# Kernel optimization log

Hardware: AMD Instinct MI355X
Metric: run time of the kernel (lower is better)

Reference implementation:

```python
import jax, jax.numpy as jnp
import numpy as np

LEARNING_RATE = 0.01


def setup_inputs() -> dict:
    key = jax.random.key(0)
    k1, k2 = jax.random.split(key)
    O, D = 512, 128  # output_dim, input_dim; batch must equal output_dim for the broadcast
    x = jax.random.normal(k1, (O, D), dtype=jnp.float32)
    weights = jax.random.normal(k2, (O, O, D), dtype=jnp.float32)
    return {"x": x, "weights": weights}


def reference(x, weights):
    # x: (B, D) with B == O; weights: (O, O, D)
    O = weights.shape[0]
    sigma = O / 2.0
    x = x.reshape(-1, weights.shape[-1])
    diff = weights - x[:, None, :]                      # (O, O, D)
    distances = jnp.sum(diff * diff, axis=-1)            # (O, O)
    winner = jnp.argmin(distances, axis=1)               # (O,)
    neighborhood = jnp.exp(-distances / (2.0 * sigma ** 2))  # (O, O)
    delta = LEARNING_RATE * neighborhood[..., None] * (x[:, None, :] - weights)  # (O, O, D)
    # torch: self.weights.data += torch.sum(delta, dim=0)  -> (O, D) broadcast over rows
    new_weights = weights + jnp.sum(delta, axis=0)        # (O, O, D)
    return winner, new_weights
```

## Files before the change

### kernel.cpp

```cpp
#include <hip/hip_runtime.h>
#include <stdint.h>

#define O_DIM 512
#define D_DIM 128
#define LR 0.01f
#define INV2SIG2 7.62939453125e-6f

typedef float f32x4 __attribute__((ext_vector_type(4)));

__global__ __launch_bounds__(256) void som_fused(
    const float* __restrict__ X,
    const float* __restrict__ W,
    float* __restrict__ dist,
    float* __restrict__ outW)
{
    const int j    = blockIdx.x;
    const int wave = threadIdx.x >> 6;
    const int lane = threadIdx.x & 63;
    const int g    = lane >> 4;
    const int i16  = lane & 15;
    const int dA   = i16 * 4;
    const int dB   = 64 + dA;

    float acc[8];
    #pragma unroll
    for (int u = 0; u < 8; ++u) acc[u] = 0.f;

    const int bbase = wave * 4 + g;

    #pragma unroll 2
    for (int k = 0; k < 32; k += 4) {
        float4 wa[4], wb[4], xa[4], xb[4];
        int bb[4];
        #pragma unroll
        for (int u = 0; u < 4; ++u) {
            bb[u] = bbase + (k + u) * 16;
            const float* wrow = W + ((size_t)bb[u] * O_DIM + j) * D_DIM;
            const float* xrow = X + (size_t)bb[u] * D_DIM;
            wa[u] = *(const float4*)(wrow + dA);
            wb[u] = *(const float4*)(wrow + dB);
            xa[u] = *(const float4*)(xrow + dA);
            xb[u] = *(const float4*)(xrow + dB);
        }
        #pragma unroll
        for (int u = 0; u < 4; ++u) {
            float dx[8];
            dx[0] = wa[u].x - xa[u].x; dx[1] = wa[u].y - xa[u].y;
            dx[2] = wa[u].z - xa[u].z; dx[3] = wa[u].w - xa[u].w;
            dx[4] = wb[u].x - xb[u].x; dx[5] = wb[u].y - xb[u].y;
            dx[6] = wb[u].z - xb[u].z; dx[7] = wb[u].w - xb[u].w;

            float s = 0.f;
            #pragma unroll
            for (int v = 0; v < 8; ++v) s = fmaf(dx[v], dx[v], s);
            s += __shfl_xor(s, 1, 64);
            s += __shfl_xor(s, 2, 64);
            s += __shfl_xor(s, 4, 64);
            s += __shfl_xor(s, 8, 64);

            if (i16 == 0) dist[(size_t)bb[u] * O_DIM + j] = s;

            const float c = LR * __expf(-s * INV2SIG2);
            #pragma unroll
            for (int v = 0; v < 8; ++v) acc[v] = fmaf(-c, dx[v], acc[v]);
        }
    }

    #pragma unroll
    for (int u = 0; u < 8; ++u) {
        acc[u] += __shfl_xor(acc[u], 16, 64);
        acc[u] += __shfl_xor(acc[u], 32, 64);
    }

    __shared__ float sacc[4][D_DIM];
    __shared__ float sS[D_DIM];
    if (g == 0) {
        #pragma unroll
        for (int u = 0; u < 4; ++u) {
            sacc[wave][dA + u] = acc[u];
            sacc[wave][dB + u] = acc[4 + u];
        }
    }
    __syncthreads();
    if (threadIdx.x < D_DIM) {
        const int d = threadIdx.x;
        sS[d] = sacc[0][d] + sacc[1][d] + sacc[2][d] + sacc[3][d];
    }
    __syncthreads();

    const f32x4 sA = *(const f32x4*)(sS + dA);
    const f32x4 sB = *(const f32x4*)(sS + dB);

    #pragma unroll 4
    for (int k = 0; k < 32; ++k) {
        const int b = bbase + k * 16;
        const size_t e = ((size_t)b * O_DIM + j) * D_DIM;
        const f32x4 w4a = *(const f32x4*)(W + e + dA);
        const f32x4 w4b = *(const f32x4*)(W + e + dB);
        __builtin_nontemporal_store(w4a + sA, (f32x4*)(outW + e + dA));
        __builtin_nontemporal_store(w4b + sB, (f32x4*)(outW + e + dB));
    }
}

__global__ __launch_bounds__(64) void som_argmin(
    const float* __restrict__ dist,
    float* __restrict__ out)
{
    const int b = blockIdx.x;
    const int lane = threadIdx.x;
    unsigned long long best = ~0ull;
    #pragma unroll
    for (int k = 0; k < 8; ++k) {
        const int jj = k * 64 + lane;
        const float s = dist[(size_t)b * O_DIM + jj];
        const unsigned long long key =
            ((unsigned long long)__float_as_uint(s) << 32) | (unsigned int)jj;
        best = key < best ? key : best;
    }
    #pragma unroll
    for (int m = 32; m >= 1; m >>= 1) {
        const unsigned long long o = __shfl_xor(best, m, 64);
        best = o < best ? o : best;
    }
    if (lane == 0) out[b] = (float)(unsigned int)(best & 0xFFFFFFFFull);
}


__global__ __launch_bounds__(256) void som_pass1_atomic(
    const float* __restrict__ X, const float* __restrict__ W,
    float* __restrict__ S, unsigned long long* __restrict__ wkey)
{
    const int j = blockIdx.x >> 2, chunk = blockIdx.x & 3;
    const int wave = threadIdx.x >> 6, lane = threadIdx.x & 63;
    const int d0 = lane * 2;
    float accx = 0.f, accy = 0.f;
    const int b_end = chunk * 128 + 128;
    for (int b = chunk * 128 + wave; b < b_end; b += 4) {
        const float2 w2 = *(const float2*)(W + ((size_t)b * O_DIM + j) * D_DIM + d0);
        const float2 x2 = *(const float2*)(X + (size_t)b * D_DIM + d0);
        const float dx = w2.x - x2.x, dy = w2.y - x2.y;
        float s = dx * dx + dy * dy;
        #pragma unroll
        for (int m = 32; m >= 1; m >>= 1) s += __shfl_xor(s, m, 64);
        if (lane == 0)
            atomicMin(&wkey[b], ((unsigned long long)__float_as_uint(s) << 32) | (unsigned)j);
        const float c = LR * __expf(-s * INV2SIG2);
        accx -= c * dx; accy -= c * dy;
    }
    __shared__ float sacc[D_DIM];
    if (threadIdx.x < D_DIM) sacc[threadIdx.x] = 0.f;
    __syncthreads();
    atomicAdd(&sacc[d0], accx); atomicAdd(&sacc[d0 + 1], accy);
    __syncthreads();
    if (threadIdx.x < D_DIM) atomicAdd(&S[(size_t)j * D_DIM + threadIdx.x], sacc[threadIdx.x]);
}

__global__ __launch_bounds__(256) void som_pass2_atomic(
    const float* __restrict__ W, const float* __restrict__ S,
    const unsigned long long* __restrict__ wkey, float* __restrict__ out)
{
    const size_t tid = (size_t)blockIdx.x * blockDim.x + threadIdx.x;
    if (tid < O_DIM) out[tid] = (float)(unsigned int)(wkey[tid] & 0xFFFFFFFFull);
    float* __restrict__ outW = out + O_DIM;
    const size_t total4 = (size_t)O_DIM * O_DIM * D_DIM / 4;
    const size_t stride = (size_t)gridDim.x * blockDim.x;
    for (size_t i = tid; i < total4; i += stride) {
        const size_t e = i * 4;
        const float4 w4 = *(const float4*)(W + e);
        const float4 s4 = *(const float4*)(S + (e & (size_t)(O_DIM * D_DIM - 1)));
        float4 o4 = {w4.x + s4.x, w4.y + s4.y, w4.z + s4.z, w4.w + s4.w};
        *(float4*)(outW + e) = o4;
    }
}

extern "C" void kernel_launch(void* const* d_in, const int* in_sizes, int n_in,
                              void* d_out, int out_size, void* d_ws, size_t ws_size,
                              hipStream_t stream)
{
    const float* X = (const float*)d_in[0];
    const float* W = (const float*)d_in[1];
    float* out = (float*)d_out;

    const size_t DIST_BYTES = (size_t)O_DIM * O_DIM * sizeof(float);

    if (ws_size >= DIST_BYTES) {
        float* dist = (float*)d_ws;
        som_fused <<<dim3(512), dim3(256), 0, stream>>>(X, W, dist, out + O_DIM);
        som_argmin<<<dim3(512), dim3(64),  0, stream>>>(dist, out);
    } else {
        float* S = (float*)d_ws;
        unsigned long long* wkey =
            (unsigned long long*)((char*)d_ws + (size_t)O_DIM * D_DIM * sizeof(float));
        hipMemsetAsync(S, 0, (size_t)O_DIM * D_DIM * sizeof(float), stream);
        hipMemsetAsync(wkey, 0xFF, (size_t)O_DIM * sizeof(unsigned long long), stream);
        som_pass1_atomic<<<dim3(2048), dim3(256), 0, stream>>>(X, W, S, wkey);
        som_pass2_atomic<<<dim3(2048), dim3(256), 0, stream>>>(W, S, wkey, out);
    }
}
```

Before: 65.58 us.

## Split fused SOM kernel into two passes over half-batch blocks, merging argmin into pass B

The single fused kernel, which ran 512 blocks, each computing distances and then writing its column, is replaced by two kernels of 1024 blocks. Each block handles half of the batch rows, and partial update sums go through a workspace buffer. The argmin is folded into the second pass rather than launched as its own kernel. This doubles the block count for better occupancy and drops a launch. The cost is that W is read once more from global memory across kernels rather than while still warm within one block.

```diff
diff --git a/kernel.cpp b/kernel.cpp
--- a/kernel.cpp
+++ b/kernel.cpp
@@ -8,13 +8,14 @@
 
 typedef float f32x4 __attribute__((ext_vector_type(4)));
 
-__global__ __launch_bounds__(256) void som_fused(
+__global__ __launch_bounds__(256) void som_passA(
     const float* __restrict__ X,
     const float* __restrict__ W,
     float* __restrict__ dist,
-    float* __restrict__ outW)
-{
-    const int j    = blockIdx.x;
+    float* __restrict__ Spart)
+{
+    const int j    = blockIdx.x >> 1;
+    const int h    = blockIdx.x & 1;
     const int wave = threadIdx.x >> 6;
     const int lane = threadIdx.x & 63;
     const int g    = lane >> 4;
@@ -26,15 +27,15 @@
     #pragma unroll
     for (int u = 0; u < 8; ++u) acc[u] = 0.f;
 
-    const int bbase = wave * 4 + g;
-
-    #pragma unroll 2
-    for (int k = 0; k < 32; k += 4) {
+    const int bbase = h * 256 + wave * 4 + g;
+
+    #pragma unroll
+    for (int kb = 0; kb < 4; ++kb) {
         float4 wa[4], wb[4], xa[4], xb[4];
         int bb[4];
         #pragma unroll
         for (int u = 0; u < 4; ++u) {
-            bb[u] = bbase + (k + u) * 16;
+            bb[u] = bbase + (kb * 4 + u) * 16;
             const float* wrow = W + ((size_t)bb[u] * O_DIM + j) * D_DIM;
             const float* xrow = X + (size_t)bb[u] * D_DIM;
             wa[u] = *(const float4*)(wrow + dA);
@@ -73,7 +74,6 @@
     }
 
     __shared__ float sacc[4][D_DIM];
-    __shared__ float sS[D_DIM];
     if (g == 0) {
         #pragma unroll
         for (int u = 0; u < 4; ++u) {
@@ -84,15 +84,56 @@
     __syncthreads();
     if (threadIdx.x < D_DIM) {
         const int d = threadIdx.x;
-        sS[d] = sacc[0][d] + sacc[1][d] + sacc[2][d] + sacc[3][d];
-    }
-    __syncthreads();
-
-    const f32x4 sA = *(const f32x4*)(sS + dA);
-    const f32x4 sB = *(const f32x4*)(sS + dB);
-
+        Spart[((size_t)j * 2 + h) * D_DIM + d] =
+            sacc[0][d] + sacc[1][d] + sacc[2][d] + sacc[3][d];
+    }
+}
+
+__global__ __launch_bounds__(256) void som_passB(
+    const float* __restrict__ W,
+    const float* __restrict__ dist,
+    const float* __restrict__ Spart,
+    float* __restrict__ out)
+{
+    const int j = blockIdx.x >> 1;
+    const int h = blockIdx.x & 1;
+    const int t = threadIdx.x;
+    float* __restrict__ outW = out + O_DIM;
+
+    if (blockIdx.x < O_DIM && t < 64) {
+        const int b = blockIdx.x;
+        unsigned long long best = ~0ull;
+        #pragma unroll
+        for (int k = 0; k < 8; ++k) {
+            const int jj = k * 64 + t;
+            const float s = dist[(size_t)b * O_DIM + jj];
+            const unsigned long long key =
+                ((unsigned long long)__float_as_uint(s) << 32) | (unsigned int)jj;
+            best = key < best ? key : best;
+        }
+        #pragma unroll
+        for (int m = 32; m >= 1; m >>= 1) {
+            const unsigned long long o = __shfl_xor(best, m, 64);
+            best = o < best ? o : best;
+        }
+        if (t == 0) out[b] = (float)(unsigned int)(best & 0xFFFFFFFFull);
+    }
+
+    const int wave = t >> 6;
+    const int lane = t & 63;
+    const int g    = lane >> 4;
+    const int i16  = lane & 15;
+    const int dA   = i16 * 4;
+    const int dB   = 64 + dA;
+
+    const float* sp0 = Spart + ((size_t)j * 2) * D_DIM;
+    const float* sp1 = sp0 + D_DIM;
+    const f32x4 sA = *(const f32x4*)(sp0 + dA) + *(const f32x4*)(sp1 + dA);
+    const f32x4 sB = *(const f32x4*)(sp0 + dB) + *(const f32x4*)(sp1 + dB);
+
+    const int bbase = h * 256 + wave * 4 + g;
     #pragma unroll 4
-    for (int k = 0; k < 32; ++k) {
+    for (int k = 0; k < 16; ++k) {
         const int b = bbase + k * 16;
         const size_t e = ((size_t)b * O_DIM + j) * D_DIM;
         const f32x4 w4a = *(const f32x4*)(W + e + dA);
@@ -100,29 +141,6 @@
         __builtin_nontemporal_store(w4a + sA, (f32x4*)(outW + e + dA));
         __builtin_nontemporal_store(w4b + sB, (f32x4*)(outW + e + dB));
     }
-}
-
-__global__ __launch_bounds__(64) void som_argmin(
-    const float* __restrict__ dist,
-    float* __restrict__ out)
-{
-    const int b = blockIdx.x;
-    const int lane = threadIdx.x;
-    unsigned long long best = ~0ull;
-    #pragma unroll
-    for (int k = 0; k < 8; ++k) {
-        const int jj = k * 64 + lane;
-        const float s = dist[(size_t)b * O_DIM + jj];
-        const unsigned long long key =
-            ((unsigned long long)__float_as_uint(s) << 32) | (unsigned int)jj;
-        best = key < best ? key : best;
-    }
-    #pragma unroll
-    for (int m = 32; m >= 1; m >>= 1) {
-        const unsigned long long o = __shfl_xor(best, m, 64);
-        best = o < best ? o : best;
-    }
-    if (lane == 0) out[b] = (float)(unsigned int)(best & 0xFFFFFFFFull);
 }
 
 
@@ -181,12 +199,14 @@
     const float* W = (const float*)d_in[1];
     float* out = (float*)d_out;
 
-    const size_t DIST_BYTES = (size_t)O_DIM * O_DIM * sizeof(float);
-
-    if (ws_size >= DIST_BYTES) {
-        float* dist = (float*)d_ws;
-        som_fused <<<dim3(512), dim3(256), 0, stream>>>(X, W, dist, out + O_DIM);
-        som_argmin<<<dim3(512), dim3(64),  0, stream>>>(dist, out);
+    const size_t DIST_BYTES  = (size_t)O_DIM * O_DIM * sizeof(float);
+    const size_t SPART_BYTES = 2ull * O_DIM * D_DIM * sizeof(float);
+
+    if (ws_size >= DIST_BYTES + SPART_BYTES) {
+        float* dist  = (float*)d_ws;
+        float* Spart = (float*)((char*)d_ws + DIST_BYTES);
+        som_passA<<<dim3(1024), dim3(256), 0, stream>>>(X, W, dist, Spart);
+        som_passB<<<dim3(1024), dim3(256), 0, stream>>>(W, dist, Spart, out);
     } else {
         float* S = (float*)d_ws;
         unsigned long long* wkey =
```

After: 67.64 us. 3.1% more time.

## Hold weight slice in registers across both passes with 1024-thread blocks

Applied to the files above, without the earlier changes.

The fused kernel now uses 1024 threads per block, and each thread loads its 16 weight vectors into registers once. Those registers feed both the distance/neighborhood pass and the final update store, so the second global read of W is gone. The cost is higher register pressure (16 f32x4 per thread) at 1024-thread blocks, which may limit occupancy, plus a larger 16-way shared reduction.

```diff
diff --git a/kernel.cpp b/kernel.cpp
--- a/kernel.cpp
+++ b/kernel.cpp
@@ -8,97 +8,73 @@
 
 typedef float f32x4 __attribute__((ext_vector_type(4)));
 
-__global__ __launch_bounds__(256) void som_fused(
+__global__ __launch_bounds__(1024) void som_fused(
     const float* __restrict__ X,
     const float* __restrict__ W,
     float* __restrict__ dist,
     float* __restrict__ outW)
 {
     const int j    = blockIdx.x;
-    const int wave = threadIdx.x >> 6;
-    const int lane = threadIdx.x & 63;
-    const int g    = lane >> 4;
-    const int i16  = lane & 15;
-    const int dA   = i16 * 4;
-    const int dB   = 64 + dA;
+    const int t    = threadIdx.x;
+    const int wave = t >> 6;
+    const int lane = t & 63;
+    const int g    = lane >> 5;
+    const int i32  = lane & 31;
+    const int d0   = i32 * 4;
+    const int brow = wave * 2 + g;
 
-    float acc[8];
+    f32x4 wv[16];
     #pragma unroll
-    for (int u = 0; u < 8; ++u) acc[u] = 0.f;
-
-    const int bbase = wave * 4 + g;
-
-    #pragma unroll 2
-    for (int k = 0; k < 32; k += 4) {
-        float4 wa[4], wb[4], xa[4], xb[4];
-        int bb[4];
-        #pragma unroll
-        for (int u = 0; u < 4; ++u) {
-            bb[u] = bbase + (k + u) * 16;
-            const float* wrow = W + ((size_t)bb[u] * O_DIM + j) * D_DIM;
-            const float* xrow = X + (size_t)bb[u] * D_DIM;
-            wa[u] = *(const float4*)(wrow + dA);
-            wb[u] = *(const float4*)(wrow + dB);
-            xa[u] = *(const float4*)(xrow + dA);
-            xb[u] = *(const float4*)(xrow + dB);
-        }
-        #pragma unroll
-        for (int u = 0; u < 4; ++u) {
-            float dx[8];
-            dx[0] = wa[u].x - xa[u].x; dx[1] = wa[u].y - xa[u].y;
-            dx[2] = wa[u].z - xa[u].z; dx[3] = wa[u].w - xa[u].w;
-            dx[4] = wb[u].x - xb[u].x; dx[5] = wb[u].y - xb[u].y;
-            dx[6] = wb[u].z - xb[u].z; dx[7] = wb[u].w - xb[u].w;
-
-            float s = 0.f;
-            #pragma unroll
-            for (int v = 0; v < 8; ++v) s = fmaf(dx[v], dx[v], s);
-            s += __shfl_xor(s, 1, 64);
-            s += __shfl_xor(s, 2, 64);
-            s += __shfl_xor(s, 4, 64);
-            s += __shfl_xor(s, 8, 64);
-
-            if (i16 == 0) dist[(size_t)bb[u] * O_DIM + j] = s;
-
-            const float c = LR * __expf(-s * INV2SIG2);
-            #pragma unroll
-            for (int v = 0; v < 8; ++v) acc[v] = fmaf(-c, dx[v], acc[v]);
-        }
+    for (int s = 0; s < 16; ++s) {
+        const int b = s * 32 + brow;
+        wv[s] = *(const f32x4*)(W + ((size_t)b * O_DIM + j) * D_DIM + d0);
     }
 
+    f32x4 acc = {0.f, 0.f, 0.f, 0.f};
     #pragma unroll
-    for (int u = 0; u < 8; ++u) {
-        acc[u] += __shfl_xor(acc[u], 16, 64);
-        acc[u] += __shfl_xor(acc[u], 32, 64);
+    for (int s = 0; s < 16; ++s) {
+        const int b = s * 32 + brow;
+        const f32x4 x4 = *(const f32x4*)(X + (size_t)b * D_DIM + d0);
+        const f32x4 dx = wv[s] - x4;
+        float sum = dx.x * dx.x;
+        sum = fmaf(dx.y, dx.y, sum);
+        sum = fmaf(dx.z, dx.z, sum);
+        sum = fmaf(dx.w, dx.w, sum);
+        sum += __shfl_xor(sum, 1, 64);
+        sum += __shfl_xor(sum, 2, 64);
+        sum += __shfl_xor(sum, 4, 64);
+        sum += __shfl_xor(sum, 8, 64);
+        sum += __shfl_xor(sum, 16, 64);
+
+        if (i32 == 0) dist[(size_t)b * O_DIM + j] = sum;
+
+        const float c = LR * __expf(-sum * INV2SIG2);
+        acc -= c * dx;
     }
 
-    __shared__ float sacc[4][D_DIM];
+    acc.x += __shfl_xor(acc.x, 32, 64);
+    acc.y += __shfl_xor(acc.y, 32, 64);
+    acc.z += __shfl_xor(acc.z, 32, 64);
+    acc.w += __shfl_xor(acc.w, 32, 64);
+
+    __shared__ float sacc[16][D_DIM];
     __shared__ float sS[D_DIM];
-    if (g == 0) {
+    if (lane < 32) *(f32x4*)(&sacc[wave][d0]) = acc;
+    __syncthreads();
+    if (t < D_DIM) {
+        float v = sacc[0][t];
         #pragma unroll
-        for (int u = 0; u < 4; ++u) {
-            sacc[wave][dA + u] = acc[u];
-            sacc[wave][dB + u] = acc[4 + u];
-        }
+        for (int w = 1; w < 16; ++w) v += sacc[w][t];
+        sS[t] = v;
     }
     __syncthreads();
-    if (threadIdx.x < D_DIM) {
-        const int d = threadIdx.x;
-        sS[d] = sacc[0][d] + sacc[1][d] + sacc[2][d] + sacc[3][d];
-    }
-    __syncthreads();
+    const f32x4 s4 = *(const f32x4*)(sS + d0);
 
-    const f32x4 sA = *(const f32x4*)(sS + dA);
-    const f32x4 sB = *(const f32x4*)(sS + dB);
-
-    #pragma unroll 4
-    for (int k = 0; k < 32; ++k) {
-        const int b = bbase + k * 16;
-        const size_t e = ((size_t)b * O_DIM + j) * D_DIM;
-        const f32x4 w4a = *(const f32x4*)(W + e + dA);
-        const f32x4 w4b = *(const f32x4*)(W + e + dB);
-        __builtin_nontemporal_store(w4a + sA, (f32x4*)(outW + e + dA));
-        __builtin_nontemporal_store(w4b + sB, (f32x4*)(outW + e + dB));
+    #pragma unroll
+    for (int s = 0; s < 16; ++s) {
+        const int b = s * 32 + brow;
+        __builtin_nontemporal_store(
+            wv[s] + s4, (f32x4*)(outW + ((size_t)b * O_DIM + j) * D_DIM + d0));
     }
 }
 
@@ -185,8 +161,8 @@
 
     if (ws_size >= DIST_BYTES) {
         float* dist = (float*)d_ws;
-        som_fused <<<dim3(512), dim3(256), 0, stream>>>(X, W, dist, out + O_DIM);
-        som_argmin<<<dim3(512), dim3(64),  0, stream>>>(dist, out);
+        som_fused <<<dim3(512), dim3(1024), 0, stream>>>(X, W, dist, out + O_DIM);
+        som_argmin<<<dim3(512), dim3(64),   0, stream>>>(dist, out);
     } else {
         float* S = (float*)d_ws;
         unsigned long long* wkey =
```

New measurement: 98.60 us. +50.3%, slower.
